# Kernel tuning notes

Measured on AMD Instinct MI355X. Metric: run time of the kernel, lower is better.

## Reference

```python
import jax, jax.numpy as jnp
import numpy as np

C = 64
TOPK = 5


def conv2d(x, w, b, pad):
    y = jax.lax.conv_general_dilated(
        x, w, window_strides=(1, 1), padding=[(pad, pad), (pad, pad)],
        dimension_numbers=('NCHW', 'OIHW', 'NCHW'))
    return y + b[None, :, None, None]


def unfold3x3_reflect(x):
    # torch: F.unfold(ReflectionPad2d(1)(x), kernel_size=3) -> [B, C*9, H*W]
    B, Cc, H, W = x.shape
    xp = jnp.pad(x, ((0, 0), (0, 0), (1, 1), (1, 1)), mode='reflect')
    patches = jnp.stack(
        [xp[:, :, kh:kh + H, kw:kw + W] for kh in range(3) for kw in range(3)],
        axis=2)  # [B, C, 9, H, W], kernel order kh*3+kw matches torch unfold
    return patches.reshape(B, Cc * 9, H * W)


def fold3x3(cols, H, W):
    # torch: F.fold(cols, (H, W), kernel_size=3, padding=1) -> overlap-add
    B, D, L = cols.shape
    Cc = D // 9
    patches = cols.reshape(B, Cc, 3, 3, H, W)
    out = jnp.zeros((B, Cc, H + 2, W + 2), cols.dtype)
    for kh in range(3):
        for kw in range(3):
            out = out.at[:, :, kh:kh + H, kw:kw + W].add(patches[:, :, kh, kw])
    return out[:, :, 1:H + 1, 1:W + 1]


def setup_inputs() -> dict:
    key = jax.random.key(0)
    ks = jax.random.split(key, 9)
    B, H, W = 4, 64, 64
    x = jax.random.normal(ks[0], (B, C, H, W), jnp.float32)
    s = 0.05
    w1 = jax.random.normal(ks[1], (C, C, 3, 3), jnp.float32) * s
    b1 = jax.random.normal(ks[2], (C,), jnp.float32) * s
    w2 = jax.random.normal(ks[3], (C, C, 3, 3), jnp.float32) * s
    b2 = jax.random.normal(ks[4], (C,), jnp.float32) * s
    wt1 = jax.random.normal(ks[5], (C, C * (TOPK - 1), 1, 1), jnp.float32) * s
    bt1 = jax.random.normal(ks[6], (C,), jnp.float32) * s
    wt2 = jax.random.normal(ks[7], (C, C * 3, 1, 1), jnp.float32) * s
    bt2 = jax.random.normal(ks[8], (C,), jnp.float32) * s
    return {'x': x, 'w1': w1, 'b1': b1, 'w2': w2, 'b2': b2,
            'wt1': wt1, 'bt1': bt1, 'wt2': wt2, 'bt2': bt2}


def reference(x, w1, b1, w2, b2, wt1, bt1, wt2, bt2):
    B, Cc, H, W = x.shape
    L = H * W
    EPS = 1e-12

    feature = conv2d(jax.nn.relu(conv2d(x, w1, b1, 1)), w2, b2, 1)

    x_unfold = unfold3x3_reflect(x)                   # [B, 9C, L]
    qn = x_unfold / jnp.maximum(
        jnp.linalg.norm(x_unfold, axis=1, keepdims=True), EPS)
    kn = qn  # q and k are both x, normalized along the feature (9C) axis

    # R_qk[b, m, l] = <k patch m, q patch l>  (torch bmm(k[B,L,D], q[B,D,L]))
    R = jnp.einsum('bdm,bdl->bml', kn, qn)            # [B, L, L]
    vals, idxs = jax.lax.top_k(R.transpose(0, 2, 1), TOPK)  # over key axis
    R_maxs = vals.transpose(0, 2, 1)                  # [B, k, L]
    R_indexs = idxs.transpose(0, 2, 1)                # [B, k, L]

    Ts = []
    for i in range(1, TOPK):
        idx = R_indexs[:, i, :]                       # [B, L]
        T_unfold = jnp.take_along_axis(x_unfold, idx[:, None, :], axis=2)
        T = fold3x3(T_unfold, H, W) / 9.0             # [B, C, H, W]
        S = R_maxs[:, i, :].reshape(B, 1, H, W)
        Ts.append(T * S)

    texture = conv2d(jnp.concatenate(Ts, axis=1), wt1, bt1, 0)
    y = conv2d(jnp.concatenate([feature, x, texture], axis=1), wt2, bt2, 0)
    return y
```

## Files before the change

### kernel.cpp

```cpp
#include <hip/hip_runtime.h>
#include <hip/hip_bf16.h>
#include <hip/hip_fp8.h>
#include <stdint.h>

typedef unsigned short ushort_t;
typedef __attribute__((ext_vector_type(8))) short short8;
typedef __attribute__((ext_vector_type(16))) float f32x16;
typedef __attribute__((ext_vector_type(8))) int i32x8;
typedef __attribute__((ext_vector_type(4))) int i32x4;

#define DEV __device__ __forceinline__

DEV int refl(int j) { return j < 0 ? -j : (j > 63 ? 126 - j : j); }

DEV void gload_lds16(const void* g, void* l) {
  __builtin_amdgcn_global_load_lds(
      (const __attribute__((address_space(1))) unsigned int*)g,
      (__attribute__((address_space(3))) unsigned int*)l, 16, 0, 0);
}

DEV unsigned packval(float v, int idx) {
  unsigned u = __float_as_uint(v);
  u ^= (0x80000000u | (unsigned)((int)u >> 31));
  return (u & 0xFFFFF000u) | (unsigned)idx;
}

DEV void ins8(unsigned (&s)[8], unsigned p) {
#pragma unroll
  for (int j = 0; j < 8; ++j) {
    unsigned mx = s[j] > p ? s[j] : p;
    unsigned mn = s[j] > p ? p : s[j];
    s[j] = mx;
    p = mn;
  }
}

DEV i32x8 ldfrag(const uint8_t* p0, const uint8_t* p1) {
  i32x4 lo = *(const i32x4*)p0;
  i32x4 hi = *(const i32x4*)p1;
  i32x8 r;
  r[0] = lo[0]; r[1] = lo[1]; r[2] = lo[2]; r[3] = lo[3];
  r[4] = hi[0]; r[5] = hi[1]; r[6] = hi[2]; r[7] = hi[3];
  return r;
}

DEV int toff(int r, int d, int rbstride) {
  return (r >> 3) * rbstride + (d >> 5) * 256 + ((d >> 3) & 3) * 64 + (r & 7) * 8 + (d & 7);
}

__global__ __launch_bounds__(256) void k_prep(
    const float* __restrict__ x, float* __restrict__ xt,
    const float* __restrict__ w1, const float* __restrict__ w2,
    const float* __restrict__ wt1, const float* __restrict__ bt1,
    const float* __restrict__ wt2, const float* __restrict__ bt2,
    ushort_t* __restrict__ Wb1t, ushort_t* __restrict__ Wb2t,
    ushort_t* __restrict__ Wcatb, float* __restrict__ beff) {
  int t = threadIdx.x;
  if (blockIdx.x < 256) {
    __shared__ float tile[64][65];
    int wg = blockIdx.x;
    int b = wg >> 6, pt = wg & 63;
    int lane = t & 63, grp = t >> 6;
    const float* xb = x + ((size_t)b * 64) * 4096 + pt * 64;
#pragma unroll
    for (int j = 0; j < 16; ++j) {
      int c = j * 4 + grp;
      tile[c][lane] = xb[(size_t)c * 4096 + lane];
    }
    __syncthreads();
    float* xtb = xt + ((size_t)b * 4096 + (size_t)pt * 64) * 64;
#pragma unroll
    for (int j = 0; j < 16; ++j) {
      int p = j * 4 + grp;
      xtb[p * 64 + lane] = tile[lane][p];
    }
    return;
  }
  int id = (blockIdx.x - 256) * 256 + t;
  if (id < 36864) {
    int n = id & 63, d = id >> 6;
    __hip_bfloat16 h = __float2bfloat16(w1[(n * 64 + (d & 63)) * 9 + (d >> 6)]);
    Wb1t[toff(n, d, 4608)] = *(ushort_t*)&h;
  } else if (id < 73728) {
    int rel = id - 36864;
    int n = rel & 63, d = rel >> 6;
    __hip_bfloat16 h = __float2bfloat16(w2[(n * 64 + (d & 63)) * 9 + (d >> 6)]);
    Wb2t[toff(n, d, 4608)] = *(ushort_t*)&h;
  } else if (id < 98304) {
    int rel = id - 73728;
    int n = rel & 63, d = rel >> 6;
    float s;
    if (d < 128) {
      s = wt2[n * 192 + d];
    } else {
      int j = d - 128;
      s = 0.f;
      for (int ct = 0; ct < 64; ++ct) s += wt2[n * 192 + 128 + ct] * wt1[ct * 256 + j];
    }
    __hip_bfloat16 h = __float2bfloat16(s);
    Wcatb[toff(n, d, 3072)] = *(ushort_t*)&h;
  } else if (id < 98368) {
    int co = id - 98304;
    float s = bt2[co];
    for (int ct = 0; ct < 64; ++ct) s += wt2[co * 192 + 128 + ct] * bt1[ct];
    beff[co] = s;
  }
}

__global__ __launch_bounds__(512) void k_unfold(const float* __restrict__ xt,
                                                uint8_t* __restrict__ Xq,
                                                double* __restrict__ dinv) {
  __shared__ uint8_t U[4608];
  int rbg = blockIdx.x;
  int b = rbg >> 9, rb = rbg & 511;
  int t = threadIdx.x;
  int p = t >> 6, lane = t & 63;
  int l = rb * 8 + p;
  int y = l >> 6, xq = l & 63;
  const float* xb = xt + ((size_t)b * 4096) * 64;
  float v[9];
  double s = 0.0;
#pragma unroll
  for (int tap = 0; tap < 9; ++tap) {
    int kh = tap / 3, kw = tap % 3;
    int gy = refl(y + kh - 1), gx = refl(xq + kw - 1);
    v[tap] = xb[(gy * 64 + gx) * 64 + lane];
    s += (double)v[tap] * (double)v[tap];
  }
#pragma unroll
  for (int off = 32; off; off >>= 1) s += __shfl_xor(s, off, 64);
  double n = sqrt(s);
  if (n < 1e-12) n = 1e-12;
  if (lane == 0) dinv[b * 4096 + l] = 1.0 / n;
  float inv = (float)(1.0 / n);
#pragma unroll
  for (int tap = 0; tap < 9; ++tap) {
    __hip_fp8_e4m3 h(v[tap] * inv);
    U[tap * 512 + (lane >> 4) * 128 + p * 16 + (lane & 15)] = h.__x;
  }
  __syncthreads();
  uint8_t* g = Xq + (size_t)rbg * 4608;
  if (t < 288) *(uint4*)&g[t * 16] = *(const uint4*)&U[t * 16];
}

__global__ __launch_bounds__(256) void k_cgemm(const float* __restrict__ in_t,
                                               const ushort_t* __restrict__ Wt,
                                               const float* __restrict__ bias,
                                               float* __restrict__ out_t,
                                               int do_relu) {
  __shared__ __align__(16) ushort_t Ab[2][2048];
  __shared__ __align__(16) ushort_t Bb[2][2048];
  int t = threadIdx.x;
  int w = t >> 6, lane = t & 63, rr = lane & 31, half = lane >> 5;
  int mi = w >> 1, ni = w & 1;
  int bid = blockIdx.x;
  int b = bid >> 6, y = bid & 63;
  const float* xrow = in_t + ((size_t)b * 4096) * 64;
  int sr = t >> 2, sq = t & 3;

  float bz = bias[ni * 32 + rr];
  f32x16 acc;
#pragma unroll
  for (int q = 0; q < 16; ++q) acc[q] = bz;

#define STAGE_CONV(kc_, buf_)                                                   \
  {                                                                             \
    int tap = (kc_) >> 1, ch = ((kc_) & 1) * 32 + sq * 8;                       \
    int kh = tap / 3, kw = tap % 3;                                             \
    int gy = y + kh - 1, gx = sr + kw - 1;                                      \
    ushort_t tmp[8];                                                            \
    if (gy >= 0 && gy < 64 && gx >= 0 && gx < 64) {                             \
      const float* src = xrow + ((size_t)(gy * 64 + gx)) * 64 + ch;             \
      float4 v0 = *(const float4*)src;                                          \
      float4 v1 = *(const float4*)(src + 4);                                    \
      float vv[8] = {v0.x, v0.y, v0.z, v0.w, v1.x, v1.y, v1.z, v1.w};           \
      _Pragma("unroll") for (int j = 0; j < 8; ++j) {                           \
        __hip_bfloat16 h = __float2bfloat16(vv[j]);                             \
        tmp[j] = *(ushort_t*)&h;                                                \
      }                                                                         \
    } else {                                                                    \
      _Pragma("unroll") for (int j = 0; j < 8; ++j) tmp[j] = 0;                 \
    }                                                                           \
    *(uint4*)&Ab[buf_][(sr >> 3) * 256 + sq * 64 + (sr & 7) * 8] = *(uint4*)tmp;\
    gload_lds16(Wt + (size_t)(t >> 5) * 4608 + (kc_) * 256 + (t & 31) * 8,      \
                &Bb[buf_][t * 8]);                                              \
  }

  STAGE_CONV(0, 0)
#pragma unroll 2
  for (int kc = 0; kc < 18; ++kc) {
    __syncthreads();
    if (kc < 17) STAGE_CONV(kc + 1, (kc + 1) & 1)
    const ushort_t* tA = Ab[kc & 1];
    const ushort_t* tB = Bb[kc & 1];
#pragma unroll
    for (int ks = 0; ks < 2; ++ks) {
      int seg8 = (ks * 2 + half) * 8 + (rr & 7);
      short8 af = *(const short8*)&tA[(mi * 4 + (rr >> 3)) * 256 + seg8 * 8];
      short8 bf = *(const short8*)&tB[(ni * 4 + (rr >> 3)) * 256 + seg8 * 8];
      acc = __builtin_amdgcn_mfma_f32_32x32x16_bf16(af, bf, acc, 0, 0, 0);
    }
  }
#undef STAGE_CONV
  float* orow = out_t + ((size_t)b * 4096 + y * 64) * 64;
  int n = ni * 32 + rr;
#pragma unroll
  for (int reg = 0; reg < 16; ++reg) {
    int m = mi * 32 + (reg & 3) + 8 * (reg >> 2) + 4 * half;
    float vv = acc[reg];
    if (do_relu) vv = fmaxf(vv, 0.f);
    orow[m * 64 + n] = vv;
  }
}

__global__ __launch_bounds__(256, 4) void k_gram(const uint8_t* __restrict__ Xq,
                                                 int* __restrict__ pidx) {
  __shared__ __align__(16) char lds[40960];
  uint8_t* sAb = (uint8_t*)lds;
  uint8_t* sBb = (uint8_t*)(lds + 32768);

  int wg = blockIdx.x;
  int u = wg & 7, v = wg >> 3;
  int bs = u + 8 * (v & 1);
  int b = bs >> 2, sp = bs & 3;
  int cb = v >> 1;
  int colbase = cb * 64;
  int t = threadIdx.x;
  int w = t >> 6, lane = t & 63;
  int rr = lane & 31, half = lane >> 5;
  int rb8 = rr >> 3, r8 = rr & 7;
  int so0 = (2 * half) * 8 + r8;
  int so1 = so0 + 8;

  const uint8_t* Xb = Xq + (size_t)b * 512 * 4608;
  const uint8_t* XB = Xb + (size_t)(cb * 8) * 4608;

  unsigned list[8];
#pragma unroll
  for (int j = 0; j < 8; ++j) list[j] = 0u;

#pragma unroll 1
  for (int mt = 0; mt < 4; ++mt) {
    int rowbase = sp * 1024 + mt * 256;
    __syncthreads();
    const uint8_t* XA = Xb + (size_t)(sp * 128 + mt * 32) * 4608;
    f32x16 acc[2][2];
#pragma unroll
    for (int im = 0; im < 2; ++im)
#pragma unroll
      for (int il = 0; il < 2; ++il)
#pragma unroll
        for (int q = 0; q < 16; ++q) acc[im][il][q] = 0.f;
    {
#pragma unroll
      for (int j = 0; j < 4; ++j) {
        int s = j * 256 + t;
        gload_lds16(XA + (size_t)(s >> 5) * 4608 + (s & 31) * 16, sAb + s * 16);
      }
      gload_lds16(XB + (size_t)(t >> 5) * 4608 + (t & 31) * 16, sBb + t * 16);
    }
#pragma unroll 1
    for (int kc = 0; kc < 9; ++kc) {
      __syncthreads();
      if (kc < 8) {
        int buf = (kc + 1) & 1;
        int ko = (kc + 1) * 512;
#pragma unroll
        for (int j = 0; j < 4; ++j) {
          int s = j * 256 + t;
          gload_lds16(XA + (size_t)(s >> 5) * 4608 + ko + (s & 31) * 16,
                      sAb + buf * 16384 + s * 16);
        }
        gload_lds16(XB + (size_t)(t >> 5) * 4608 + ko + (t & 31) * 16,
                    sBb + buf * 4096 + t * 16);
      }
      const uint8_t* tA = sAb + (kc & 1) * 16384;
      const uint8_t* tB = sBb + (kc & 1) * 4096;
      i32x8 af[2], bf[2];
#pragma unroll
      for (int im = 0; im < 2; ++im) {
        int rbA = w * 8 + im * 4 + rb8;
        af[im] = ldfrag(&tA[(rbA * 32 + so0) * 16], &tA[(rbA * 32 + so1) * 16]);
      }
#pragma unroll
      for (int il = 0; il < 2; ++il) {
        int rbB = il * 4 + rb8;
        bf[il] = ldfrag(&tB[(rbB * 32 + so0) * 16], &tB[(rbB * 32 + so1) * 16]);
      }
      acc[0][0] = __builtin_amdgcn_mfma_scale_f32_32x32x64_f8f6f4(
          af[0], bf[0], acc[0][0], 0, 0, 0, 0x7F7F7F7F, 0, 0x7F7F7F7F);
      acc[0][1] = __builtin_amdgcn_mfma_scale_f32_32x32x64_f8f6f4(
          af[0], bf[1], acc[0][1], 0, 0, 0, 0x7F7F7F7F, 0, 0x7F7F7F7F);
      acc[1][0] = __builtin_amdgcn_mfma_scale_f32_32x32x64_f8f6f4(
          af[1], bf[0], acc[1][0], 0, 0, 0, 0x7F7F7F7F, 0, 0x7F7F7F7F);
      acc[1][1] = __builtin_amdgcn_mfma_scale_f32_32x32x64_f8f6f4(
          af[1], bf[1], acc[1][1], 0, 0, 0, 0x7F7F7F7F, 0, 0x7F7F7F7F);
    }
    int rowb = rowbase + w * 64;
#pragma unroll
    for (int im = 0; im < 2; ++im) {
#pragma unroll
      for (int reg = 0; reg < 16; ++reg) {
        float a0 = acc[im][0][reg], a1 = acc[im][1][reg];
        float vo = half ? a1 : a0;
        float vs = half ? a0 : a1;
        float vr = __shfl_xor(vs, 32, 64);
        int rbase = rowb + im * 32 + (reg & 3) + 8 * (reg >> 2);
        ins8(list, packval(vo, rbase + 4 * half));
        ins8(list, packval(vr, rbase + 4 * (1 - half)));
      }
    }
  }
  __syncthreads();
  unsigned* M = (unsigned*)lds;
#pragma unroll
  for (int j = 0; j < 8; ++j) M[lane * 33 + w * 8 + j] = list[j];
  __syncthreads();
  if (t < 64) {
    unsigned bl[8];
#pragma unroll
    for (int j = 0; j < 8; ++j) bl[j] = 0u;
#pragma unroll 1
    for (int i = 0; i < 32; ++i) ins8(bl, M[t * 33 + i]);
    size_t base = (((size_t)b * 4 + sp) * 4096 + colbase + t) * 8;
#pragma unroll
    for (int j = 0; j < 8; ++j) pidx[base + j] = (int)bl[j];
  }
}

__global__ __launch_bounds__(256) void k_refine(const float* __restrict__ xt,
                                                const double* __restrict__ dinv,
                                                const int* __restrict__ pidx,
                                                float* __restrict__ Sval,
                                                int* __restrict__ Sidx) {
  int w = threadIdx.x >> 6, lane = threadIdx.x & 63;
  int gl = blockIdx.x * 4 + w;
  int b = gl >> 12, l = gl & 4095;
  int y = l >> 6, xq = l & 63;
  const float* xb = xt + ((size_t)b * 4096) * 64;
  unsigned cp = 0u;
  if (lane < 32) {
    int sp = lane >> 3, j = lane & 7;
    cp = (unsigned)pidx[(((size_t)b * 4 + sp) * 4096 + l) * 8 + j];
  }
  int wm[8];
#pragma unroll
  for (int r = 0; r < 8; ++r) {
    unsigned v = cp;
#pragma unroll
    for (int off = 32; off; off >>= 1) {
      unsigned ov = __shfl_xor(v, off, 64);
      v = ov > v ? ov : v;
    }
    wm[r] = (int)(v & 4095u);
    if (cp == v) cp = 0u;
  }
  int ch4 = (lane & 15) * 4;
  float4 xl4[9];
#pragma unroll
  for (int tap = 0; tap < 9; ++tap) {
    int kh = tap / 3, kw = tap % 3;
    xl4[tap] = *(const float4*)&xb[(refl(y + kh - 1) * 64 + refl(xq + kw - 1)) * 64 + ch4];
  }
  double il = dinv[b * 4096 + l];
  double rv = -1e30;
  int ridx = 0x7fffffff;
#pragma unroll
  for (int it = 0; it < 2; ++it) {
    int m = wm[it * 4 + (lane >> 4)];
    int my = m >> 6, mx = m & 63;
    double d = 0.0;
#pragma unroll
    for (int tap = 0; tap < 9; ++tap) {
      int kh = tap / 3, kw = tap % 3;
      float4 gv = *(const float4*)&xb[(refl(my + kh - 1) * 64 + refl(mx + kw - 1)) * 64 + ch4];
      d += (double)xl4[tap].x * (double)gv.x + (double)xl4[tap].y * (double)gv.y +
           (double)xl4[tap].z * (double)gv.z + (double)xl4[tap].w * (double)gv.w;
    }
#pragma unroll
    for (int off = 1; off < 16; off <<= 1) d += __shfl_xor(d, off, 64);
    double R = d * il * dinv[b * 4096 + m];
    double Rsrc = __shfl(R, (lane & 3) * 16, 64);
    int msrc = __shfl(m, (lane & 3) * 16, 64);
    if ((lane >> 2) == it && lane < 8) { rv = Rsrc; ridx = msrc; }
  }
#pragma unroll
  for (int r = 0; r < 5; ++r) {
    double v = rv;
    int i = ridx;
#pragma unroll
    for (int off = 32; off; off >>= 1) {
      double ov = __shfl_xor(v, off, 64);
      int oi = __shfl_xor(i, off, 64);
      if (ov > v || (ov == v && oi < i)) { v = ov; i = oi; }
    }
    if (r >= 1 && lane == 0) {
      Sval[((size_t)b * 5 + r) * 4096 + l] = (float)v;
      Sidx[((size_t)b * 5 + r) * 4096 + l] = i;
    }
    if (rv == v && ridx == i) rv = -1e30;
  }
}

__global__ __launch_bounds__(256, 4) void k_tex(const float* __restrict__ xt,
                                                const float* __restrict__ feat,
                                                const float* __restrict__ Sval,
                                                const int* __restrict__ Sidx,
                                                ushort_t* __restrict__ Xb16) {
  __shared__ ushort_t U[6144];
  __shared__ int SI[3 * 18 * 4];
  __shared__ float SV[16 * 4];
  int t = threadIdx.x;
  int w = t >> 6, lane = t & 63;
  int p0 = blockIdx.x * 16;
  int b = p0 >> 12, pl = p0 & 4095;
  int y0 = pl >> 6, x0 = pl & 63;
  if (t < 216) {
    int r = t / 72, rem = t % 72;
    int c = rem >> 2, i = (rem & 3) + 1;
    int qy = y0 - 1 + r, qx = x0 - 1 + c;
    int m = 0x7fffffff;
    if (qy >= 0 && qy < 64 && qx >= 0 && qx < 64)
      m = Sidx[((size_t)b * 5 + i) * 4096 + qy * 64 + qx] & 4095;
    SI[(r * 18 + c) * 4 + (i - 1)] = m;
  }
  if (t < 64) {
    int px = t >> 2, i = (t & 3) + 1;
    SV[px * 4 + (i - 1)] = Sval[((size_t)b * 5 + i) * 4096 + pl + px];
  }
#pragma unroll
  for (int jj = 0; jj < 4; ++jj) {
    int px = w * 4 + jj;
    float fv = feat[((size_t)b * 4096 + pl + px) * 64 + lane];
    float xv = xt[((size_t)b * 4096 + pl + px) * 64 + lane];
    __hip_bfloat16 hf = __float2bfloat16(fv);
    __hip_bfloat16 hx = __float2bfloat16(xv);
    U[toff(px, lane, 3072)] = *(ushort_t*)&hf;
    U[toff(px, 64 + lane, 3072)] = *(ushort_t*)&hx;
  }
  __syncthreads();
  const float* xb = xt + ((size_t)b * 4096) * 64;
#pragma unroll 4
  for (int k = 0; k < 16; ++k) {
    int pr = w * 16 + k;
    int px = pr >> 2, i = pr & 3;
    float a = 0.f;
#pragma unroll
    for (int tap = 0; tap < 9; ++tap) {
      int kh = tap / 3, kw = tap % 3;
      int m = SI[((2 - kh) * 18 + px + 2 - kw) * 4 + i];
      if (m != 0x7fffffff) {
        int gy = refl((m >> 6) + kh - 1), gx = refl((m & 63) + kw - 1);
        a += xb[(gy * 64 + gx) * 64 + lane];
      }
    }
    __hip_bfloat16 h = __float2bfloat16(a * SV[px * 4 + i] * (1.f / 9.f));
    U[toff(px, 128 + i * 64 + lane, 3072)] = *(ushort_t*)&h;
  }
  __syncthreads();
  ushort_t* g = Xb16 + (size_t)blockIdx.x * 6144;
#pragma unroll
  for (int i = 0; i < 3; ++i) {
    int s = i * 256 + t;
    *(uint4*)&g[s * 8] = *(const uint4*)&U[s * 8];
  }
}

__global__ __launch_bounds__(256) void k_outg(const ushort_t* __restrict__ Xb16,
                                              const ushort_t* __restrict__ Wcatb,
                                              const float* __restrict__ beff,
                                              float* __restrict__ out) {
  __shared__ __align__(16) ushort_t Ab[2][2048];
  __shared__ __align__(16) ushort_t Bb[2][2048];
  __shared__ float T[64 * 65];
  int t = threadIdx.x;
  int w = t >> 6, lane = t & 63, rr = lane & 31, half = lane >> 5;
  int mi = w >> 1, ni = w & 1;
  int bid = blockIdx.x;
  int b = bid >> 6, y = bid & 63;
  const ushort_t* XA = Xb16 + (size_t)bid * 24576;

  float bz = beff[ni * 32 + rr];
  f32x16 acc;
#pragma unroll
  for (int q = 0; q < 16; ++q) acc[q] = bz;

#define STAGE_OUT(kc_, buf_)                                                    \
  {                                                                             \
    gload_lds16(XA + (size_t)(t >> 5) * 3072 + (kc_) * 256 + (t & 31) * 8,      \
                &Ab[buf_][t * 8]);                                              \
    gload_lds16(Wcatb + (size_t)(t >> 5) * 3072 + (kc_) * 256 + (t & 31) * 8,   \
                &Bb[buf_][t * 8]);                                              \
  }

  STAGE_OUT(0, 0)
#pragma unroll 2
  for (int kc = 0; kc < 12; ++kc) {
    __syncthreads();
    if (kc < 11) STAGE_OUT(kc + 1, (kc + 1) & 1)
    const ushort_t* tA = Ab[kc & 1];
    const ushort_t* tB = Bb[kc & 1];
#pragma unroll
    for (int ks = 0; ks < 2; ++ks) {
      int seg8 = (ks * 2 + half) * 8 + (rr & 7);
      short8 af = *(const short8*)&tA[(mi * 4 + (rr >> 3)) * 256 + seg8 * 8];
      short8 bf = *(const short8*)&tB[(ni * 4 + (rr >> 3)) * 256 + seg8 * 8];
      acc = __builtin_amdgcn_mfma_f32_32x32x16_bf16(af, bf, acc, 0, 0, 0);
    }
  }
#undef STAGE_OUT
  __syncthreads();
  int n = ni * 32 + rr;
#pragma unroll
  for (int reg = 0; reg < 16; ++reg) {
    int m = mi * 32 + (reg & 3) + 8 * (reg >> 2) + 4 * half;
    T[m * 65 + n] = acc[reg];
  }
  __syncthreads();
  int n2 = t >> 2, grp = t & 3;
  float o[16];
#pragma unroll
  for (int j = 0; j < 16; ++j) o[j] = T[(grp * 16 + j) * 65 + n2];
  float* od = out + ((size_t)b * 64 + n2) * 4096 + y * 64 + grp * 16;
#pragma unroll
  for (int j = 0; j < 4; ++j) *(float4*)(od + j * 4) = *(float4*)&o[j * 4];
}

extern "C" void kernel_launch(void* const* d_in, const int* in_sizes, int n_in,
                              void* d_out, int out_size, void* d_ws, size_t ws_size,
                              hipStream_t stream) {
  const float* x = (const float*)d_in[0];
  const float* w1 = (const float*)d_in[1];
  const float* b1 = (const float*)d_in[2];
  const float* w2 = (const float*)d_in[3];
  const float* b2 = (const float*)d_in[4];
  const float* wt1 = (const float*)d_in[5];
  const float* bt1 = (const float*)d_in[6];
  const float* wt2 = (const float*)d_in[7];
  const float* bt2 = (const float*)d_in[8];

  char* ws = (char*)d_ws;
  float* x_t = (float*)(ws + 0);
  float* y1 = (float*)(ws + 4194304);
  float* feat = (float*)(ws + 8388608);
  uint8_t* Xq = (uint8_t*)(ws + 12582912);
  ushort_t* Xb16 = (ushort_t*)(ws + 12582912);
  double* dinv = (double*)(ws + 31457280);
  int* pidx = (int*)(ws + 31653888);
  float* Sval = (float*)(ws + 33751040);
  int* Sidx = (int*)(ws + 34078720);
  ushort_t* Wb1t = (ushort_t*)(ws + 34406400);
  ushort_t* Wb2t = (ushort_t*)(ws + 34553856);
  ushort_t* Wcatb = (ushort_t*)(ws + 34701312);
  float* beff = (float*)(ws + 34799616);
  float* out = (float*)d_out;

  k_prep<<<dim3(641), dim3(256), 0, stream>>>(x, x_t, w1, w2, wt1, bt1, wt2, bt2,
                                              Wb1t, Wb2t, Wcatb, beff);
  k_unfold<<<dim3(2048), dim3(512), 0, stream>>>(x_t, Xq, dinv);
  k_cgemm<<<dim3(256), dim3(256), 0, stream>>>(x_t, Wb1t, b1, y1, 1);
  k_cgemm<<<dim3(256), dim3(256), 0, stream>>>(y1, Wb2t, b2, feat, 0);
  k_gram<<<dim3(1024), dim3(256), 0, stream>>>(Xq, pidx);
  k_refine<<<dim3(4096), dim3(256), 0, stream>>>(x_t, dinv, pidx, Sval, Sidx);
  k_tex<<<dim3(1024), dim3(256), 0, stream>>>(x_t, feat, Sval, Sidx, Xb16);
  k_outg<<<dim3(256), dim3(256), 0, stream>>>(Xb16, Wcatb, beff, out);
}
```

Before: 278.6 us.

## Merge unfold into first conv launch, shrink texture blocks, simplify top-k key packing

The patch-unfold/normalize kernel and the first 3x3 conv GEMM become one launch. Block index selects which body runs, and the unfold body now uses 256 threads handling two patches each. The texture kernel now handles 8 pixels per block instead of 16, with a higher occupancy hint, to get more parallelism and lower LDS use. The sortable key packing for top-k replaces the sign-flip transform with adding 2.0, which relies on similarities being in [-1,1] and slightly changes mantissa truncation.

```diff
diff --git a/kernel.cpp b/kernel.cpp
--- a/kernel.cpp
+++ b/kernel.cpp
@@ -20,9 +20,7 @@
 }
 
 DEV unsigned packval(float v, int idx) {
-  unsigned u = __float_as_uint(v);
-  u ^= (0x80000000u | (unsigned)((int)u >> 31));
-  return (u & 0xFFFFF000u) | (unsigned)idx;
+  return (__float_as_uint(v + 2.0f) & 0xFFFFF000u) | (unsigned)idx;
 }
 
 DEV void ins8(unsigned (&s)[8], unsigned p) {
@@ -107,53 +105,13 @@
   }
 }
 
-__global__ __launch_bounds__(512) void k_unfold(const float* __restrict__ xt,
-                                                uint8_t* __restrict__ Xq,
-                                                double* __restrict__ dinv) {
-  __shared__ uint8_t U[4608];
-  int rbg = blockIdx.x;
-  int b = rbg >> 9, rb = rbg & 511;
-  int t = threadIdx.x;
-  int p = t >> 6, lane = t & 63;
-  int l = rb * 8 + p;
-  int y = l >> 6, xq = l & 63;
-  const float* xb = xt + ((size_t)b * 4096) * 64;
-  float v[9];
-  double s = 0.0;
-#pragma unroll
-  for (int tap = 0; tap < 9; ++tap) {
-    int kh = tap / 3, kw = tap % 3;
-    int gy = refl(y + kh - 1), gx = refl(xq + kw - 1);
-    v[tap] = xb[(gy * 64 + gx) * 64 + lane];
-    s += (double)v[tap] * (double)v[tap];
-  }
-#pragma unroll
-  for (int off = 32; off; off >>= 1) s += __shfl_xor(s, off, 64);
-  double n = sqrt(s);
-  if (n < 1e-12) n = 1e-12;
-  if (lane == 0) dinv[b * 4096 + l] = 1.0 / n;
-  float inv = (float)(1.0 / n);
-#pragma unroll
-  for (int tap = 0; tap < 9; ++tap) {
-    __hip_fp8_e4m3 h(v[tap] * inv);
-    U[tap * 512 + (lane >> 4) * 128 + p * 16 + (lane & 15)] = h.__x;
-  }
-  __syncthreads();
-  uint8_t* g = Xq + (size_t)rbg * 4608;
-  if (t < 288) *(uint4*)&g[t * 16] = *(const uint4*)&U[t * 16];
-}
-
-__global__ __launch_bounds__(256) void k_cgemm(const float* __restrict__ in_t,
-                                               const ushort_t* __restrict__ Wt,
-                                               const float* __restrict__ bias,
-                                               float* __restrict__ out_t,
-                                               int do_relu) {
-  __shared__ __align__(16) ushort_t Ab[2][2048];
-  __shared__ __align__(16) ushort_t Bb[2][2048];
-  int t = threadIdx.x;
+DEV void conv_body(char* smem, int bid, const float* __restrict__ in_t,
+                   const ushort_t* __restrict__ Wt, const float* __restrict__ bias,
+                   float* __restrict__ out_t, int do_relu, int t) {
+  ushort_t* Ab = (ushort_t*)smem;
+  ushort_t* Bb = (ushort_t*)(smem + 8192);
   int w = t >> 6, lane = t & 63, rr = lane & 31, half = lane >> 5;
   int mi = w >> 1, ni = w & 1;
-  int bid = blockIdx.x;
   int b = bid >> 6, y = bid & 63;
   const float* xrow = in_t + ((size_t)b * 4096) * 64;
   int sr = t >> 2, sq = t & 3;
@@ -181,9 +139,10 @@
     } else {                                                                    \
       _Pragma("unroll") for (int j = 0; j < 8; ++j) tmp[j] = 0;                 \
     }                                                                           \
-    *(uint4*)&Ab[buf_][(sr >> 3) * 256 + sq * 64 + (sr & 7) * 8] = *(uint4*)tmp;\
+    *(uint4*)&Ab[(buf_)*2048 + (sr >> 3) * 256 + sq * 64 + (sr & 7) * 8] =      \
+        *(uint4*)tmp;                                                           \
     gload_lds16(Wt + (size_t)(t >> 5) * 4608 + (kc_) * 256 + (t & 31) * 8,      \
-                &Bb[buf_][t * 8]);                                              \
+                &Bb[(buf_)*2048 + t * 8]);                                      \
   }
 
   STAGE_CONV(0, 0)
@@ -191,8 +150,8 @@
   for (int kc = 0; kc < 18; ++kc) {
     __syncthreads();
     if (kc < 17) STAGE_CONV(kc + 1, (kc + 1) & 1)
-    const ushort_t* tA = Ab[kc & 1];
-    const ushort_t* tB = Bb[kc & 1];
+    const ushort_t* tA = Ab + (kc & 1) * 2048;
+    const ushort_t* tB = Bb + (kc & 1) * 2048;
 #pragma unroll
     for (int ks = 0; ks < 2; ++ks) {
       int seg8 = (ks * 2 + half) * 8 + (rr & 7);
@@ -211,6 +170,64 @@
     if (do_relu) vv = fmaxf(vv, 0.f);
     orow[m * 64 + n] = vv;
   }
+}
+
+__global__ __launch_bounds__(256) void k_fuseA(
+    const float* __restrict__ xt, uint8_t* __restrict__ Xq,
+    double* __restrict__ dinv, const ushort_t* __restrict__ Wb1t,
+    const float* __restrict__ b1, float* __restrict__ y1) {
+  __shared__ __align__(16) char smem[16384];
+  int t = threadIdx.x;
+  if (blockIdx.x >= 2048) {
+    conv_body(smem, blockIdx.x - 2048, xt, Wb1t, b1, y1, 1, t);
+    return;
+  }
+  uint8_t* U = (uint8_t*)smem;
+  int rbg = blockIdx.x;
+  int b = rbg >> 9, rb = rbg & 511;
+  int wv = t >> 6, lane = t & 63;
+  const float* xb = xt + ((size_t)b * 4096) * 64;
+#pragma unroll
+  for (int pp = 0; pp < 2; ++pp) {
+    int p = wv * 2 + pp;
+    int l = rb * 8 + p;
+    int y = l >> 6, xq = l & 63;
+    float v[9];
+    double s = 0.0;
+#pragma unroll
+    for (int tap = 0; tap < 9; ++tap) {
+      int kh = tap / 3, kw = tap % 3;
+      int gy = refl(y + kh - 1), gx = refl(xq + kw - 1);
+      v[tap] = xb[(gy * 64 + gx) * 64 + lane];
+      s += (double)v[tap] * (double)v[tap];
+    }
+#pragma unroll
+    for (int off = 32; off; off >>= 1) s += __shfl_xor(s, off, 64);
+    double n = sqrt(s);
+    if (n < 1e-12) n = 1e-12;
+    if (lane == 0) dinv[b * 4096 + l] = 1.0 / n;
+    float inv = (float)(1.0 / n);
+#pragma unroll
+    for (int tap = 0; tap < 9; ++tap) {
+      __hip_fp8_e4m3 h(v[tap] * inv);
+      U[tap * 512 + (lane >> 4) * 128 + p * 16 + (lane & 15)] = h.__x;
+    }
+  }
+  __syncthreads();
+  uint8_t* g = Xq + (size_t)rbg * 4608;
+  {
+    *(uint4*)&g[t * 16] = *(const uint4*)&U[t * 16];
+    if (t < 32) *(uint4*)&g[(256 + t) * 16] = *(const uint4*)&U[(256 + t) * 16];
+  }
+}
+
+__global__ __launch_bounds__(256) void k_cgemm(const float* __restrict__ in_t,
+                                               const ushort_t* __restrict__ Wt,
+                                               const float* __restrict__ bias,
+                                               float* __restrict__ out_t,
+                                               int do_relu) {
+  __shared__ __align__(16) char smem[16384];
+  conv_body(smem, blockIdx.x, in_t, Wt, bias, out_t, do_relu, threadIdx.x);
 }
 
 __global__ __launch_bounds__(256, 4) void k_gram(const uint8_t* __restrict__ Xq,
@@ -402,35 +419,35 @@
   }
 }
 
-__global__ __launch_bounds__(256, 4) void k_tex(const float* __restrict__ xt,
+__global__ __launch_bounds__(256, 8) void k_tex(const float* __restrict__ xt,
                                                 const float* __restrict__ feat,
                                                 const float* __restrict__ Sval,
                                                 const int* __restrict__ Sidx,
                                                 ushort_t* __restrict__ Xb16) {
-  __shared__ ushort_t U[6144];
-  __shared__ int SI[3 * 18 * 4];
-  __shared__ float SV[16 * 4];
+  __shared__ ushort_t U[3072];
+  __shared__ int SI[3 * 10 * 4];
+  __shared__ float SV[8 * 4];
   int t = threadIdx.x;
   int w = t >> 6, lane = t & 63;
-  int p0 = blockIdx.x * 16;
+  int p0 = blockIdx.x * 8;
   int b = p0 >> 12, pl = p0 & 4095;
   int y0 = pl >> 6, x0 = pl & 63;
-  if (t < 216) {
-    int r = t / 72, rem = t % 72;
+  if (t < 120) {
+    int r = t / 40, rem = t % 40;
     int c = rem >> 2, i = (rem & 3) + 1;
     int qy = y0 - 1 + r, qx = x0 - 1 + c;
     int m = 0x7fffffff;
     if (qy >= 0 && qy < 64 && qx >= 0 && qx < 64)
       m = Sidx[((size_t)b * 5 + i) * 4096 + qy * 64 + qx] & 4095;
-    SI[(r * 18 + c) * 4 + (i - 1)] = m;
-  }
-  if (t < 64) {
+    SI[(r * 10 + c) * 4 + (i - 1)] = m;
+  }
+  if (t < 32) {
     int px = t >> 2, i = (t & 3) + 1;
     SV[px * 4 + (i - 1)] = Sval[((size_t)b * 5 + i) * 4096 + pl + px];
   }
 #pragma unroll
-  for (int jj = 0; jj < 4; ++jj) {
-    int px = w * 4 + jj;
+  for (int jj = 0; jj < 2; ++jj) {
+    int px = w * 2 + jj;
     float fv = feat[((size_t)b * 4096 + pl + px) * 64 + lane];
     float xv = xt[((size_t)b * 4096 + pl + px) * 64 + lane];
     __hip_bfloat16 hf = __float2bfloat16(fv);
@@ -440,15 +457,15 @@
   }
   __syncthreads();
   const float* xb = xt + ((size_t)b * 4096) * 64;
-#pragma unroll 4
-  for (int k = 0; k < 16; ++k) {
-    int pr = w * 16 + k;
+#pragma unroll 8
+  for (int k = 0; k < 8; ++k) {
+    int pr = w * 8 + k;
     int px = pr >> 2, i = pr & 3;
     float a = 0.f;
 #pragma unroll
     for (int tap = 0; tap < 9; ++tap) {
       int kh = tap / 3, kw = tap % 3;
-      int m = SI[((2 - kh) * 18 + px + 2 - kw) * 4 + i];
+      int m = SI[((2 - kh) * 10 + px + 2 - kw) * 4 + i];
       if (m != 0x7fffffff) {
         int gy = refl((m >> 6) + kh - 1), gx = refl((m & 63) + kw - 1);
         a += xb[(gy * 64 + gx) * 64 + lane];
@@ -458,11 +475,10 @@
     U[toff(px, 128 + i * 64 + lane, 3072)] = *(ushort_t*)&h;
   }
   __syncthreads();
-  ushort_t* g = Xb16 + (size_t)blockIdx.x * 6144;
-#pragma unroll
-  for (int i = 0; i < 3; ++i) {
-    int s = i * 256 + t;
-    *(uint4*)&g[s * 8] = *(const uint4*)&U[s * 8];
+  ushort_t* g = Xb16 + (size_t)blockIdx.x * 3072;
+  {
+    *(uint4*)&g[t * 8] = *(const uint4*)&U[t * 8];
+    if (t < 128) *(uint4*)&g[(256 + t) * 8] = *(const uint4*)&U[(256 + t) * 8];
   }
 }
 
@@ -557,11 +573,10 @@
 
   k_prep<<<dim3(641), dim3(256), 0, stream>>>(x, x_t, w1, w2, wt1, bt1, wt2, bt2,
                                               Wb1t, Wb2t, Wcatb, beff);
-  k_unfold<<<dim3(2048), dim3(512), 0, stream>>>(x_t, Xq, dinv);
-  k_cgemm<<<dim3(256), dim3(256), 0, stream>>>(x_t, Wb1t, b1, y1, 1);
+  k_fuseA<<<dim3(2304), dim3(256), 0, stream>>>(x_t, Xq, dinv, Wb1t, b1, y1);
   k_cgemm<<<dim3(256), dim3(256), 0, stream>>>(y1, Wb2t, b2, feat, 0);
   k_gram<<<dim3(1024), dim3(256), 0, stream>>>(Xq, pidx);
   k_refine<<<dim3(4096), dim3(256), 0, stream>>>(x_t, dinv, pidx, Sval, Sidx);
-  k_tex<<<dim3(1024), dim3(256), 0, stream>>>(x_t, feat, Sval, Sidx, Xb16);
+  k_tex<<<dim3(2048), dim3(256), 0, stream>>>(x_t, feat, Sval, Sidx, Xb16);
   k_outg<<<dim3(256), dim3(256), 0, stream>>>(Xb16, Wcatb, beff, out);
 }
```

Result: faster. 255.2 us (-8.4%).
